# Kernel optimization log

Measured on AMD Instinct MI355X. Metric: run time of the kernel, lower is better.

The kernel has to match this reference:

```python
import jax, jax.numpy as jnp
import numpy as np

NUM_HEADS = 16


def setup_inputs() -> dict:
    key = jax.random.key(0)
    ks = jax.random.split(key, 7)
    dim, hd = 1024, 64
    B, H, W = 64, 14, 14  # B = batch * num_windows, 14x14 window
    x = jax.random.normal(ks[0], (B, H, W, dim), dtype=jnp.float32)
    qkv_w = jax.random.normal(ks[1], (dim, 3 * dim), dtype=jnp.float32) * (dim ** -0.5)
    qkv_b = jnp.zeros((3 * dim,), dtype=jnp.float32)
    proj_w = jax.random.normal(ks[2], (dim, dim), dtype=jnp.float32) * (dim ** -0.5)
    proj_b = jnp.zeros((dim,), dtype=jnp.float32)
    rel_pos_h = jax.random.normal(ks[3], (2 * H - 1, hd), dtype=jnp.float32) * 0.02
    rel_pos_w = jax.random.normal(ks[4], (2 * W - 1, hd), dtype=jnp.float32) * 0.02
    return {"x": x, "qkv_w": qkv_w, "qkv_b": qkv_b, "proj_w": proj_w,
            "proj_b": proj_b, "rel_pos_h": rel_pos_h, "rel_pos_w": rel_pos_w}


def reference(x, qkv_w, qkv_b, proj_w, proj_b, rel_pos_h, rel_pos_w):
    B, H, W, dim = x.shape
    nH = NUM_HEADS
    hd = dim // nH
    scale = hd ** -0.5

    # qkv projection: [B, HW, 3*dim]
    qkv = x.reshape(B, H * W, dim) @ qkv_w + qkv_b
    # -> [3, nH, B, HW, hd] -> [3, nH*B, HW, hd]
    qkv = qkv.reshape(B, H * W, 3, nH, hd).transpose(2, 3, 0, 1, 4)
    qkv = qkv.reshape(3, nH * B, H * W, hd)
    q, k, v = qkv[0], qkv[1], qkv[2]

    # scaled QK^T: [nH*B, HW, HW]
    attn = jnp.einsum('bqc,bkc->bqk', q * scale, k)

    # decomposed relative position bias (q_size == k_size, no interpolation)
    Rh = rel_pos_h[jnp.arange(H)[:, None] - jnp.arange(H)[None, :] + (H - 1)]  # [H,H,hd]
    Rw = rel_pos_w[jnp.arange(W)[:, None] - jnp.arange(W)[None, :] + (W - 1)]  # [W,W,hd]
    r_q = q.reshape(nH * B, H, W, hd)
    rel_h = jnp.einsum('bhwc,hkc->bhwk', r_q, Rh)  # [nH*B,H,W,H]
    rel_w = jnp.einsum('bhwc,wkc->bhwk', r_q, Rw)  # [nH*B,H,W,W]
    attn = (attn.reshape(nH * B, H, W, H, W)
            + rel_h[:, :, :, :, None]
            + rel_w[:, :, :, None, :]).reshape(nH * B, H * W, H * W)

    attn = jax.nn.softmax(attn, axis=-1)
    out = attn @ v  # [nH*B, HW, hd]

    # merge heads: [nH,B,H,W,hd] -> [B,H,W,dim]
    out = out.reshape(nH, B, H, W, hd).transpose(1, 2, 3, 0, 4).reshape(B, H, W, dim)
    return out @ proj_w + proj_b
```

## Files before the change

### kernel.cpp

```cpp
#include <hip/hip_runtime.h>
#include <cstdint>
#include <cstddef>

typedef unsigned short u16;
typedef unsigned int u32;
typedef float f32x4 __attribute__((ext_vector_type(4)));
typedef short short8 __attribute__((ext_vector_type(8)));
typedef u32 u32x2 __attribute__((ext_vector_type(2)));

#define HW 196
#define DIM 1024
#define HD 64
#define SP 208
#define SPV 224
#define NBH 1024

__device__ __forceinline__ float bf2f(u16 x){
  union { u32 u; float f; } c; c.u = ((u32)x) << 16; return c.f;
}
__device__ __forceinline__ u16 f2bf(float f){
  union { float f; u32 u; } c; c.f = f;
  return (u16)((c.u + 0x7fffu + ((c.u >> 16) & 1u)) >> 16);
}
__device__ __forceinline__ u32 cvtpk_bf16(float lo, float hi){
  u32 r;
  asm("v_cvt_pk_bf16_f32 %0, %1, %2" : "=v"(r) : "v"(lo), "v"(hi));
  return r;
}
#define LGKM_FENCE() do { \
    asm volatile("s_waitcnt lgkmcnt(0)" ::: "memory"); \
    __builtin_amdgcn_sched_barrier(0); \
  } while (0)
#define DS_FENCE() do { \
    asm volatile("s_waitcnt lgkmcnt(0)" ::: "memory"); \
    __builtin_amdgcn_sched_barrier(0x7F); \
  } while (0)
#define WAITV4() asm volatile("s_waitcnt vmcnt(4)" ::: "memory")
#define BAR() __builtin_amdgcn_s_barrier()

typedef __attribute__((address_space(3))) void lds_void_t;
typedef __attribute__((address_space(1))) const void glb_void_t;
__device__ __forceinline__ void gload_lds16(const void* g, void* l){
  __builtin_amdgcn_global_load_lds((glb_void_t*)g, (lds_void_t*)l, 16, 0, 0);
}

__global__ __launch_bounds__(256) void k_prep(const float* __restrict__ x,
    u16* __restrict__ xb,
    const float* __restrict__ qkv_w, u16* __restrict__ wqkvT,
    const float* __restrict__ proj_w, u16* __restrict__ wprojT,
    const float* __restrict__ rph, const float* __restrict__ rpw,
    u16* __restrict__ rphb, u16* __restrict__ rpwb)
{
  __shared__ float t[32][33];
  int blk = blockIdx.x;
  if (blk < 6272){
    int i = blk * 256 + threadIdx.x;
    const f32x4* p = (const f32x4*)(x + (size_t)i * 8);
    f32x4 v0 = p[0], v1 = p[1];
    short8 tt;
    #pragma unroll
    for (int e = 0; e < 4; ++e){
      tt[e]   = (short)f2bf(v0[e]);
      tt[4+e] = (short)f2bf(v1[e]);
    }
    *(short8*)(xb + (size_t)i * 8) = tt;
  } else if (blk < 10368){
    const float* w; u16* wT; int K = 1024, N; int idx;
    if (blk < 9344){ w = qkv_w; wT = wqkvT; N = 3072; idx = blk - 6272; }
    else           { w = proj_w; wT = wprojT; N = 1024; idx = blk - 9344; }
    int nb = N >> 5;
    int n0 = (idx % nb) * 32, k0 = (idx / nb) * 32;
    int c = threadIdx.x & 31, rr = threadIdx.x >> 5;
    #pragma unroll
    for (int i = 0; i < 4; ++i){
      int r = rr + i*8;
      t[r][c] = w[(size_t)(k0 + r) * N + n0 + c];
    }
    __syncthreads();
    #pragma unroll
    for (int i = 0; i < 4; ++i){
      int r = rr + i*8;
      wT[(size_t)(n0 + r) * K + k0 + c] = f2bf(t[c][r]);
    }
  } else {
    int r = threadIdx.x >> 3, cc = (threadIdx.x & 7) * 8;
    #pragma unroll
    for (int tsel = 0; tsel < 2; ++tsel){
      const float* src = tsel ? rpw : rph;
      u16* dst = tsel ? rpwb : rphb;
      short8 v;
      #pragma unroll
      for (int e = 0; e < 8; ++e)
        v[e] = (r < 27) ? (short)f2bf(src[(size_t)r * 64 + cc + e]) : (short)0;
      *(short8*)(dst + (size_t)r * 64 + cc) = v;
    }
  }
}

template<int MODE>
__global__ __launch_bounds__(512, 2) void k_g256(const u16* __restrict__ Ab,
    const u16* __restrict__ Bt, const float* __restrict__ bias,
    u16* __restrict__ qg, u16* __restrict__ kg, u16* __restrict__ vTg,
    float* __restrict__ outf, int K, int N, int ntm, int ntn)
{
  extern __shared__ __align__(16) u16 smem[];
  const int tid = threadIdx.x;
  const int lane = tid & 63, wv = tid >> 6;
  const int wr = wv >> 2, wc = wv & 3;
  const int l16 = lane & 15, lk = lane >> 4;

  const int nwg = ntm * ntn;
  int bid = blockIdx.x;
  int q8 = nwg >> 3, r8 = nwg & 7;
  int xcd = bid & 7, loc = bid >> 3;
  int wgid = (xcd < r8 ? xcd*(q8+1) : r8*(q8+1) + (xcd - r8)*q8) + loc;
  int gsz = 8 * ntn;
  int g = wgid / gsz, rem = wgid - g * gsz;
  int gm = ntm - g * 8; if (gm > 8) gm = 8;
  int ry = g * 8 + rem % gm;
  int cy = rem / gm;
  const size_t m0 = (size_t)ry * 256;
  const size_t n0 = (size_t)cy * 256;
  const int nk = K >> 6;

  auto off = [&](int d, int ab, int ks){ return ((d*2 + ab)*2 + ks) * 8192; };

  auto stageH = [&](int d, int ab, int ks, int tile){
    const u16* src = ab ? Bt : Ab;
    size_t rb = ab ? n0 : m0;
    int c = (lane & 3) ^ ((lane >> 3) & 3);
    #pragma unroll
    for (int i = 0; i < 2; ++i){
      int rh = 32*wv + 16*i + (lane >> 2);
      gload_lds16(src + (rb + rh) * (size_t)K + tile*64 + ks*32 + c*8,
                  smem + off(d, ab, ks) + (32*wv + 16*i) * 32);
    }
  };
  auto ldA = [&](short8* a, int d, int ks, int h){
    #pragma unroll
    for (int m2 = 0; m2 < 4; ++m2){
      int r = wr*128 + h*64 + m2*16 + l16;
      a[m2] = *(const short8*)(smem + off(d,0,ks) + r*32 + ((lk ^ ((r>>1)&3)) << 3));
    }
  };
  auto ldB = [&](short8* b, int d, int ks){
    #pragma unroll
    for (int ni = 0; ni < 4; ++ni){
      int r = wc*64 + ni*16 + l16;
      b[ni] = *(const short8*)(smem + off(d,1,ks) + r*32 + ((lk ^ ((r>>1)&3)) << 3));
    }
  };

  f32x4 acc[8][4] = {};
  auto mm = [&](int h, short8* a, short8* b){
    __builtin_amdgcn_s_setprio(1);
    #pragma unroll
    for (int m2 = 0; m2 < 4; ++m2)
      #pragma unroll
      for (int ni = 0; ni < 4; ++ni)
        acc[h*4+m2][ni] = __builtin_amdgcn_mfma_f32_16x16x32_bf16(b[ni], a[m2], acc[h*4+m2][ni], 0, 0, 0);
    __builtin_amdgcn_s_setprio(0);
  };

  stageH(0, 0, 0, 0); stageH(0, 1, 0, 0); stageH(0, 0, 1, 0); stageH(0, 1, 1, 0);
  WAITV4(); BAR();

  #pragma unroll 1
  for (int kt = 0; kt < nk; ++kt){
    const int d = kt & 1, dn = d ^ 1;
    const int tn = (kt + 1 < nk) ? kt + 1 : nk - 1;
    short8 a[4], b0[4], b1[4];
    ldA(a, d, 0, 0); ldB(b0, d, 0);
    stageH(dn, 0, 0, tn);
    BAR(); LGKM_FENCE();
    mm(0, a, b0);
    BAR();
    ldA(a, d, 0, 1);
    stageH(dn, 1, 0, tn);
    WAITV4();
    BAR(); LGKM_FENCE();
    mm(1, a, b0);
    BAR();
    ldA(a, d, 1, 0); ldB(b1, d, 1);
    stageH(dn, 0, 1, tn);
    BAR(); LGKM_FENCE();
    mm(0, a, b1);
    BAR();
    ldA(a, d, 1, 1);
    stageH(dn, 1, 1, tn);
    WAITV4();
    BAR(); LGKM_FENCE();
    mm(1, a, b1);
    BAR();
  }

  const int rowb = (int)m0 + wr*128;
  const int colb = (int)n0 + wc*64;
  if constexpr (MODE == 1){
    #pragma unroll
    for (int mi = 0; mi < 8; ++mi){
      int r = rowb + mi*16 + l16;
      float* orow = outf + (size_t)r * N;
      #pragma unroll
      for (int ni = 0; ni < 4; ++ni){
        int c0 = colb + ni*16 + lk*4;
        f32x4 bz = *(const f32x4*)(bias + c0);
        f32x4 v = acc[mi][ni] + bz;
        *(f32x4*)(orow + c0) = v;
      }
    }
  } else {
    const int t3 = colb >> 10;
    if (t3 < 2){
      u16* dst0 = (t3 == 0) ? qg : kg;
      const float sc = (t3 == 0) ? 1.0f : 0.125f;
      #pragma unroll
      for (int mi = 0; mi < 8; ++mi){
        int r = rowb + mi*16 + l16;
        int b = r / 196, n = r - b * 196;
        #pragma unroll
        for (int ni = 0; ni < 4; ++ni){
          int rr2 = ((colb & 1023) + ni*16);
          int hh = rr2 >> 6, ccb = (rr2 & 63) + lk*4;
          const float* bz = bias + colb + ni*16 + lk*4;
          u32 w0 = cvtpk_bf16((acc[mi][ni][0] + bz[0])*sc, (acc[mi][ni][1] + bz[1])*sc);
          u32 w1 = cvtpk_bf16((acc[mi][ni][2] + bz[2])*sc, (acc[mi][ni][3] + bz[3])*sc);
          u32* dst = (u32*)(dst0 + ((size_t)(hh*64 + b) * SP + n) * HD + ccb);
          dst[0] = w0; dst[1] = w1;
        }
      }
    } else {
      #pragma unroll
      for (int mi = 0; mi < 8; ++mi){
        int r = rowb + mi*16 + l16;
        int b = r / 196, n = r - b * 196;
        #pragma unroll
        for (int ni = 0; ni < 4; ++ni){
          int col0 = colb + ni*16 + lk*4;
          f32x4 bz = *(const f32x4*)(bias + col0);
          int rem2 = col0 & 1023;
          int hh = rem2 >> 6, cc0 = rem2 & 63;
          u16* base = vTg + ((size_t)(hh*64 + b) * HD + cc0) * SPV + n;
          #pragma unroll
          for (int i = 0; i < 4; ++i)
            base[(size_t)i * SPV] = f2bf(acc[mi][ni][i] + bz[i]);
        }
      }
    }
  }
}

#define KSTR 144
#define VSTR 464
#define PWB  7424
__global__ __launch_bounds__(832, 1) void k_attn(
    const u16* __restrict__ qg, const u16* __restrict__ kg, const u16* __restrict__ vTg,
    const u16* __restrict__ rphb, const u16* __restrict__ rpwb,
    u16* __restrict__ ao)
{
  extern __shared__ __align__(16) char asmem[];
  char* Klds = asmem;
  char* Vlds = asmem + 29952;
  const int tid = threadIdx.x, lane = tid & 63, wvi = tid >> 6;
  const int l16 = lane & 15, lk = lane >> 4;
  char*  wbase = asmem + 59648 + wvi * PWB;
  float* relT  = (float*)wbase;
  u32*   Pp    = (u32*)wbase;

  const int bh = blockIdx.x;
  const int hh = bh >> 6, bb = bh & 63;
  const u16* qb = qg  + (size_t)bh * SP * HD;
  const u16* kb = kg  + (size_t)bh * SP * HD;
  const u16* vb = vTg + (size_t)bh * HD * SPV;

  for (int c = tid; c < 1664; c += 832){
    int row = c >> 3, colb = (c & 7) << 4;
    short8 d = *(const short8*)((const char*)kb + row*128 + colb);
    *(short8*)(Klds + row*KSTR + colb) = d;
  }
  for (int c = tid; c < 1792; c += 832){
    int row = c / 28, colb = (c - row*28) << 4;
    short8 d = *(const short8*)((const char*)vb + row*448 + colb);
    *(short8*)(Vlds + row*VSTR + colb) = d;
  }
  __syncthreads();

  const int mt = wvi;
  const short8 a0 = *(const short8*)(qb + (size_t)(mt*16 + l16) * HD + lk*8);
  const short8 a1 = *(const short8*)(qb + (size_t)(mt*16 + l16) * HD + 32 + lk*8);

  {
    f32x4 z = {0.f,0.f,0.f,0.f};
    f32x4 racc[2][2] = {{z,z},{z,z}};
    #pragma unroll
    for (int dt = 0; dt < 2; ++dt){
      short8 h0 = *(const short8*)(rphb + (size_t)(dt*16 + l16) * 64 + lk*8);
      short8 h1 = *(const short8*)(rphb + (size_t)(dt*16 + l16) * 64 + 32 + lk*8);
      short8 w0 = *(const short8*)(rpwb + (size_t)(dt*16 + l16) * 64 + lk*8);
      short8 w1 = *(const short8*)(rpwb + (size_t)(dt*16 + l16) * 64 + 32 + lk*8);
      racc[0][dt] = __builtin_amdgcn_mfma_f32_16x16x32_bf16(h0, a0, racc[0][dt], 0, 0, 0);
      racc[0][dt] = __builtin_amdgcn_mfma_f32_16x16x32_bf16(h1, a1, racc[0][dt], 0, 0, 0);
      racc[1][dt] = __builtin_amdgcn_mfma_f32_16x16x32_bf16(w0, a0, racc[1][dt], 0, 0, 0);
      racc[1][dt] = __builtin_amdgcn_mfma_f32_16x16x32_bf16(w1, a1, racc[1][dt], 0, 0, 0);
    }
    #pragma unroll
    for (int t = 0; t < 2; ++t)
      #pragma unroll
      for (int dt = 0; dt < 2; ++dt)
        *(f32x4*)(relT + l16*68 + t*32 + dt*16 + lk*4) = racc[t][dt];
  }
  DS_FENCE();

  int qr = mt*16 + l16;
  int qrc = qr > HW-1 ? HW-1 : qr;
  int qh = qrc / 14, qw = qrc - 14*qh;
  const float* rrow = relT + l16*68;
  const int dh0 = qh + 13, dw0 = 32 + qw + 13;
  const int lk4 = lk*4;

  f32x4 sacc[13];
  #pragma unroll
  for (int nt = 0; nt < 13; ++nt){
    #pragma unroll
    for (int i = 0; i < 4; ++i){
      int k = nt*16 + lk4 + i;
      int kh = (k * 4682) >> 16;
      if (nt == 12 && kh > 13) kh = 13;
      int kw = k - kh*14;
      float bias = rrow[dh0 - kh] + rrow[dw0 - kw];
      sacc[nt][i] = (nt == 12 && lk != 0) ? -1e30f : bias;
    }
  }

  #pragma unroll
  for (int nt = 0; nt < 13; ++nt){
    int row = nt*16 + l16;
    short8 b0 = *(const short8*)(Klds + row*KSTR + lk*16);
    short8 b1 = *(const short8*)(Klds + row*KSTR + 64 + lk*16);
    sacc[nt] = __builtin_amdgcn_mfma_f32_16x16x32_bf16(b0, a0, sacc[nt], 0, 0, 0);
    sacc[nt] = __builtin_amdgcn_mfma_f32_16x16x32_bf16(b1, a1, sacc[nt], 0, 0, 0);
  }

  float m;
  {
    float t0[13];
    #pragma unroll
    for (int nt = 0; nt < 13; ++nt)
      t0[nt] = fmaxf(fmaxf(sacc[nt][0], sacc[nt][1]), fmaxf(sacc[nt][2], sacc[nt][3]));
    float a01 = fmaxf(t0[0], t0[1]),  a23 = fmaxf(t0[2], t0[3]);
    float a45 = fmaxf(t0[4], t0[5]),  a67 = fmaxf(t0[6], t0[7]);
    float a89 = fmaxf(t0[8], t0[9]),  aab = fmaxf(t0[10], t0[11]);
    m = fmaxf(fmaxf(fmaxf(a01, a23), fmaxf(a45, a67)), fmaxf(fmaxf(a89, aab), t0[12]));
  }
  m = fmaxf(m, __shfl_xor(m, 16, 64));
  m = fmaxf(m, __shfl_xor(m, 32, 64));
  float sum;
  {
    float s4[13];
    #pragma unroll
    for (int nt = 0; nt < 13; ++nt){
      #pragma unroll
      for (int i = 0; i < 4; ++i)
        sacc[nt][i] = __expf(sacc[nt][i] - m);
      s4[nt] = (sacc[nt][0] + sacc[nt][1]) + (sacc[nt][2] + sacc[nt][3]);
    }
    float b01 = s4[0]+s4[1], b23 = s4[2]+s4[3], b45 = s4[4]+s4[5];
    float b67 = s4[6]+s4[7], b89 = s4[8]+s4[9], bab = s4[10]+s4[11];
    sum = ((b01+b23) + (b45+b67)) + ((b89+bab) + s4[12]);
  }
  sum += __shfl_xor(sum, 16, 64);
  sum += __shfl_xor(sum, 32, 64);
  float inv = 1.0f / sum;

  DS_FENCE();
  u32* prow = Pp + l16*116;
  #pragma unroll
  for (int nt = 0; nt < 13; ++nt){
    u32x2 wpk;
    wpk[0] = cvtpk_bf16(sacc[nt][0], sacc[nt][1]);
    wpk[1] = cvtpk_bf16(sacc[nt][2], sacc[nt][3]);
    *(u32x2*)(prow + nt*8 + lk*2) = wpk;
  }
  { u32x2 zz = {0u, 0u}; *(u32x2*)(prow + 104 + lk*2) = zz; }
  DS_FENCE();

  f32x4 z = {0.f,0.f,0.f,0.f};
  f32x4 oacc[4] = {z,z,z,z};
  #pragma unroll
  for (int kt = 0; kt < 7; ++kt){
    short8 pa = *(const short8*)(prow + kt*16 + lk4);
    #pragma unroll
    for (int dt = 0; dt < 4; ++dt){
      short8 bv = *(const short8*)(Vlds + (dt*16 + l16)*VSTR + kt*64 + lk*16);
      oacc[dt] = __builtin_amdgcn_mfma_f32_16x16x32_bf16(bv, pa, oacc[dt], 0, 0, 0);
    }
  }
  int qrow = mt*16 + l16;
  if (qrow < HW){
    u16* orow = ao + ((size_t)bb * HW + qrow) * DIM + hh * HD;
    #pragma unroll
    for (int dt = 0; dt < 4; ++dt){
      u32 lo = cvtpk_bf16(oacc[dt][0]*inv, oacc[dt][1]*inv);
      u32 hi = cvtpk_bf16(oacc[dt][2]*inv, oacc[dt][3]*inv);
      u32* dst = (u32*)(orow + dt*16 + lk4);
      dst[0] = lo; dst[1] = hi;
    }
  }
}

extern "C" void kernel_launch(void* const* d_in, const int* in_sizes, int n_in,
                              void* d_out, int out_size, void* d_ws, size_t ws_size,
                              hipStream_t stream)
{
  const float* x      = (const float*)d_in[0];
  const float* qkv_w  = (const float*)d_in[1];
  const float* qkv_b  = (const float*)d_in[2];
  const float* proj_w = (const float*)d_in[3];
  const float* proj_b = (const float*)d_in[4];
  const float* rph    = (const float*)d_in[5];
  const float* rpw    = (const float*)d_in[6];
  float* out = (float*)d_out;
  char* ws = (char*)d_ws;

  size_t off = 0;
  auto alloc = [&](size_t b){ size_t r = off; off += (b + 255) & ~(size_t)255; return r; };
  u16* wqkvT = (u16*)(ws + alloc((size_t)3072*1024*2));
  u16* wprojT= (u16*)(ws + alloc((size_t)1024*1024*2));
  u16* qg    = (u16*)(ws + alloc((size_t)NBH*SP*HD*2));
  u16* kg    = (u16*)(ws + alloc((size_t)NBH*SP*HD*2));
  u16* vTg   = (u16*)(ws + alloc((size_t)NBH*HD*SPV*2));
  u16* rphb  = (u16*)(ws + alloc((size_t)32*64*2));
  u16* rpwb  = (u16*)(ws + alloc((size_t)32*64*2));
  u16* xb    = (u16*)(ws + alloc((size_t)12544*1024*2));
  u16* ao    = xb;

  hipFuncSetAttribute((const void*)k_g256<0>, hipFuncAttributeMaxDynamicSharedMemorySize, 131072);
  hipFuncSetAttribute((const void*)k_g256<1>, hipFuncAttributeMaxDynamicSharedMemorySize, 131072);
  hipFuncSetAttribute((const void*)k_attn,    hipFuncAttributeMaxDynamicSharedMemorySize, 156160);

  k_prep<<<10369, 256, 0, stream>>>(x, xb, qkv_w, wqkvT, proj_w, wprojT,
                                    rph, rpw, rphb, rpwb);
  k_g256<0><<<49*12, 512, 131072, stream>>>(xb, wqkvT, qkv_b, qg, kg, vTg, nullptr,
                                            1024, 3072, 49, 12);
  k_attn<<<1024, 832, 156160, stream>>>(qg, kg, vTg, rphb, rpwb, ao);
  k_g256<1><<<49*4, 512, 131072, stream>>>(ao, wprojT, proj_b, nullptr, nullptr, nullptr, out,
                                           1024, 1024, 49, 4);
}
```

Measured before the change: 215.3 us.

## Deepen GEMM LDS staging to a 9-slot ring buffer with more prefetch

Replaces the double-buffered LDS staging in the 256x256 GEMM kernel with a 9-slot ring of quarter-tile stages, prefetching 7 stages ahead and waiting with vmcnt(6) instead of vmcnt(4). This keeps more global loads in flight so K-loop MFMA work waits less on memory latency. It raises dynamic LDS from 128 KB to 144 KB per workgroup and adds modular slot arithmetic in the loop.

```diff
diff --git a/kernel.cpp b/kernel.cpp
--- a/kernel.cpp
+++ b/kernel.cpp
@@ -35,7 +35,7 @@
     asm volatile("s_waitcnt lgkmcnt(0)" ::: "memory"); \
     __builtin_amdgcn_sched_barrier(0x7F); \
   } while (0)
-#define WAITV4() asm volatile("s_waitcnt vmcnt(4)" ::: "memory")
+#define WAITV6() asm volatile("s_waitcnt vmcnt(6)" ::: "memory")
 #define BAR() __builtin_amdgcn_s_barrier()
 
 typedef __attribute__((address_space(3))) void lds_void_t;
@@ -122,32 +122,35 @@
   const size_t m0 = (size_t)ry * 256;
   const size_t n0 = (size_t)cy * 256;
   const int nk = K >> 6;
-
-  auto off = [&](int d, int ab, int ks){ return ((d*2 + ab)*2 + ks) * 8192; };
-
-  auto stageH = [&](int d, int ab, int ks, int tile){
+  const int ntot = nk << 2;
+
+  auto stageS = [&](int s){
+    int se = s;
+    if (se >= ntot) se = ntot - 4 + (se & 3);
+    int slot = (s >= ntot ? s : se) % 9;
+    int tile = se >> 2, h = se & 3;
+    int ab = h & 1, ks = h >> 1;
     const u16* src = ab ? Bt : Ab;
     size_t rb = ab ? n0 : m0;
     int c = (lane & 3) ^ ((lane >> 3) & 3);
     #pragma unroll
     for (int i = 0; i < 2; ++i){
-      int rh = 32*wv + 16*i + (lane >> 2);
-      gload_lds16(src + (rb + rh) * (size_t)K + tile*64 + ks*32 + c*8,
-                  smem + off(d, ab, ks) + (32*wv + 16*i) * 32);
+      gload_lds16(src + (rb + 32*wv + 16*i + (lane >> 2)) * (size_t)K + tile*64 + ks*32 + c*8,
+                  smem + slot*8192 + (32*wv + 16*i) * 32);
     }
   };
-  auto ldA = [&](short8* a, int d, int ks, int h){
+  auto ldA = [&](short8* a, int slot, int h){
     #pragma unroll
     for (int m2 = 0; m2 < 4; ++m2){
       int r = wr*128 + h*64 + m2*16 + l16;
-      a[m2] = *(const short8*)(smem + off(d,0,ks) + r*32 + ((lk ^ ((r>>1)&3)) << 3));
+      a[m2] = *(const short8*)(smem + slot*8192 + r*32 + ((lk ^ ((r>>1)&3)) << 3));
     }
   };
-  auto ldB = [&](short8* b, int d, int ks){
+  auto ldB = [&](short8* b, int slot){
     #pragma unroll
     for (int ni = 0; ni < 4; ++ni){
       int r = wc*64 + ni*16 + l16;
-      b[ni] = *(const short8*)(smem + off(d,1,ks) + r*32 + ((lk ^ ((r>>1)&3)) << 3));
+      b[ni] = *(const short8*)(smem + slot*8192 + r*32 + ((lk ^ ((r>>1)&3)) << 3));
     }
   };
 
@@ -162,36 +165,42 @@
     __builtin_amdgcn_s_setprio(0);
   };
 
-  stageH(0, 0, 0, 0); stageH(0, 1, 0, 0); stageH(0, 0, 1, 0); stageH(0, 1, 1, 0);
-  WAITV4(); BAR();
-
+  #pragma unroll
+  for (int s = 0; s < 7; ++s) stageS(s);
+  WAITV6(); BAR();
+
+  int rs = 0;
+  int ss = 7;
   #pragma unroll 1
   for (int kt = 0; kt < nk; ++kt){
-    const int d = kt & 1, dn = d ^ 1;
-    const int tn = (kt + 1 < nk) ? kt + 1 : nk - 1;
+    int r0 = rs;
+    int r1 = rs+1 < 9 ? rs+1 : rs-8;
+    int r2 = rs+2 < 9 ? rs+2 : rs-7;
+    int r3 = rs+3 < 9 ? rs+3 : rs-6;
     short8 a[4], b0[4], b1[4];
-    ldA(a, d, 0, 0); ldB(b0, d, 0);
-    stageH(dn, 0, 0, tn);
+    ldA(a, r0, 0); ldB(b0, r1);
+    stageS(ss); ++ss;
     BAR(); LGKM_FENCE();
     mm(0, a, b0);
     BAR();
-    ldA(a, d, 0, 1);
-    stageH(dn, 1, 0, tn);
-    WAITV4();
+    ldA(a, r0, 1);
+    stageS(ss); ++ss;
+    WAITV6();
     BAR(); LGKM_FENCE();
     mm(1, a, b0);
     BAR();
-    ldA(a, d, 1, 0); ldB(b1, d, 1);
-    stageH(dn, 0, 1, tn);
+    ldA(a, r2, 0); ldB(b1, r3);
+    stageS(ss); ++ss;
     BAR(); LGKM_FENCE();
     mm(0, a, b1);
     BAR();
-    ldA(a, d, 1, 1);
-    stageH(dn, 1, 1, tn);
-    WAITV4();
+    ldA(a, r2, 1);
+    stageS(ss); ++ss;
+    WAITV6();
     BAR(); LGKM_FENCE();
     mm(1, a, b1);
     BAR();
+    rs = rs+4 < 9 ? rs+4 : rs-5;
   }
 
   const int rowb = (int)m0 + wr*128;
@@ -434,15 +443,15 @@
   u16* xb    = (u16*)(ws + alloc((size_t)12544*1024*2));
   u16* ao    = xb;
 
-  hipFuncSetAttribute((const void*)k_g256<0>, hipFuncAttributeMaxDynamicSharedMemorySize, 131072);
-  hipFuncSetAttribute((const void*)k_g256<1>, hipFuncAttributeMaxDynamicSharedMemorySize, 131072);
+  hipFuncSetAttribute((const void*)k_g256<0>, hipFuncAttributeMaxDynamicSharedMemorySize, 147456);
+  hipFuncSetAttribute((const void*)k_g256<1>, hipFuncAttributeMaxDynamicSharedMemorySize, 147456);
   hipFuncSetAttribute((const void*)k_attn,    hipFuncAttributeMaxDynamicSharedMemorySize, 156160);
 
   k_prep<<<10369, 256, 0, stream>>>(x, xb, qkv_w, wqkvT, proj_w, wprojT,
                                     rph, rpw, rphb, rpwb);
-  k_g256<0><<<49*12, 512, 131072, stream>>>(xb, wqkvT, qkv_b, qg, kg, vTg, nullptr,
+  k_g256<0><<<49*12, 512, 147456, stream>>>(xb, wqkvT, qkv_b, qg, kg, vTg, nullptr,
                                             1024, 3072, 49, 12);
   k_attn<<<1024, 832, 156160, stream>>>(qg, kg, vTg, rphb, rpwb, ao);
-  k_g256<1><<<49*4, 512, 131072, stream>>>(ao, wprojT, proj_b, nullptr, nullptr, nullptr, out,
+  k_g256<1><<<49*4, 512, 147456, stream>>>(ao, wprojT, proj_b, nullptr, nullptr, nullptr, out,
                                            1024, 1024, 49, 4);
 }
```

Result: slower. 237.0 us (+10.1%).
